# Kernel optimization log

Measured on AMD Instinct MI355X. Metric: run time of the kernel, lower is better.

Reference implementation:

```python
import jax, jax.numpy as jnp
import numpy as np

KEEP_RATIO = 0.5
B, H, W = 8, 1024, 1024


def setup_inputs() -> dict:
    key = jax.random.key(0)
    k1, k2, k3 = jax.random.split(key, 3)
    logits = jax.random.normal(k1, (B, 1, H, W), dtype=jnp.float32)
    targets = jax.random.randint(k2, (B, 1, H, W), 0, 2, dtype=jnp.int32)
    tissue_mask = jax.random.randint(k3, (B, 1, H, W), 0, 2, dtype=jnp.int32)
    return {"logits": logits, "targets": targets, "tissue_mask": tissue_mask}


def reference(logits, targets, tissue_mask):
    b = logits.shape[0]
    x = logits.reshape(b, -1)                       # (B, N)
    t = targets.reshape(b, -1).astype(x.dtype)      # {0,1}
    m = tissue_mask.reshape(b, -1).astype(x.dtype)  # {0,1}
    n = x.shape[1]

    # stable binary_cross_entropy_with_logits, reduction='none'
    bce = jnp.maximum(x, 0.0) - x * t + jnp.log1p(jnp.exp(-jnp.abs(x)))
    loss = bce * m                                  # masked per-pixel loss

    pos = t * m                                     # positives inside tissue
    neg = (1.0 - t) * m                             # negatives inside tissue
    n_pos = jnp.sum(pos, axis=1)                    # (B,)
    n_neg = jnp.sum(neg, axis=1)

    k_all = max(1, int(n * KEEP_RATIO))             # static python int
    # kept count per row: all positives + top-(k_all - n_pos) negatives (clamped)
    k_keep = n_pos + jnp.minimum(jnp.maximum(k_all - n_pos, 0.0), n_neg)  # (B,)

    BIG = jnp.asarray(1e30, x.dtype)
    # sort key: positives always first, then negatives by loss, then non-tissue
    sort_key = jnp.where(pos > 0, BIG, jnp.where(neg > 0, loss, -BIG))
    order = jnp.argsort(-sort_key, axis=1)          # descending
    sorted_loss = jnp.take_along_axis(loss, order, axis=1)

    ranks = jnp.arange(n, dtype=x.dtype)
    keep = (ranks[None, :] < k_keep[:, None]).astype(x.dtype)
    per_sample = jnp.sum(sorted_loss * keep, axis=1) / jnp.maximum(k_keep, 1.0)
    # fallback when no tissue pixels at all: torch keeps index 0 (loss there is 0)
    per_sample = jnp.where(k_keep > 0, per_sample, loss[:, 0])
    return jnp.mean(per_sample)
```

## Files before the change

### kernel.cpp

```cpp
#include <hip/hip_runtime.h>
#include <cstdint>
#include <cstddef>

#define N_PIX   1048576
#define B_ROWS  8
#define K_ALL   524288
#define WG_PER_ROW 256
#define ITERS   4
#define L1_BINS 4096
#define CAP     131072u

struct RowParams {
    double   sumPos;
    unsigned mode;
    unsigned T1;
    unsigned Kp;
    unsigned kneg;
    unsigned npos;
    unsigned pad;
};


__device__ void suffix_select_cnt(const unsigned* cnt, int nbins, unsigned K,
                                  unsigned (&sc)[2][256], int* res_bin, unsigned* res_cntgt)
{
    const int tid = threadIdx.x;
    const int per = nbins >> 8;
    unsigned pc = 0;
    for (int i = 0; i < per; ++i) pc += cnt[nbins - 1 - (tid * per + i)];
    int pp = 0;
    sc[0][tid] = pc;
    __syncthreads();
    for (int ofs = 1; ofs < 256; ofs <<= 1) {
        unsigned c = sc[pp][tid];
        if (tid >= ofs) c += sc[pp][tid - ofs];
        sc[pp ^ 1][tid] = c; pp ^= 1;
        __syncthreads();
    }
    unsigned inc = sc[pp][tid];
    unsigned exc = inc - pc;
    if (exc < K && K <= inc) {
        unsigned cum = exc;
        for (int i = 0; i < per; ++i) {
            int bin = nbins - 1 - (tid * per + i);
            unsigned c = cnt[bin];
            if (cum + c >= K) { *res_bin = bin; *res_cntgt = cum; break; }
            cum += c;
        }
    }
    __syncthreads();
}

__device__ void suffix_select(const unsigned* cnt, const float* sum, int nbins, unsigned K,
                              unsigned (&sc)[2][256], float (&ss)[2][256],
                              int* res_bin, unsigned* res_cntgt, float* res_sumgt)
{
    const int tid = threadIdx.x;
    const int per = nbins >> 8;
    unsigned pc = 0; float ps = 0.f;
    for (int i = 0; i < per; ++i) {
        int bin = nbins - 1 - (tid * per + i);
        pc += cnt[bin]; ps += sum[bin];
    }
    int pp = 0;
    sc[0][tid] = pc; ss[0][tid] = ps;
    __syncthreads();
    for (int ofs = 1; ofs < 256; ofs <<= 1) {
        unsigned c = sc[pp][tid]; float s = ss[pp][tid];
        if (tid >= ofs) { c += sc[pp][tid - ofs]; s += ss[pp][tid - ofs]; }
        sc[pp ^ 1][tid] = c; ss[pp ^ 1][tid] = s;
        pp ^= 1;
        __syncthreads();
    }
    unsigned inc = sc[pp][tid]; float incs = ss[pp][tid];
    unsigned exc = inc - pc;    float exs  = incs - ps;
    if (exc < K && K <= inc) {
        unsigned cum = exc; float csum = exs;
        for (int i = 0; i < per; ++i) {
            int bin = nbins - 1 - (tid * per + i);
            unsigned c = cnt[bin];
            if (cum + c >= K) { *res_bin = bin; *res_cntgt = cum; *res_sumgt = csum; break; }
            cum += c; csum += sum[bin];
        }
    }
    __syncthreads();
}

__global__ __launch_bounds__(256, 4) void k_pass1(
    const float4* __restrict__ lg, const int4* __restrict__ tg, const int4* __restrict__ mk,
    uint4* __restrict__ keybuf, unsigned* __restrict__ histCnt,
    unsigned* __restrict__ partNpos, unsigned* __restrict__ partNneg, double* __restrict__ partSpos)
{
    __shared__ unsigned hc[L1_BINS];
    __shared__ unsigned swp[4], swn[4];
    __shared__ double   sws[4];
    const int tid = threadIdx.x;
    for (int b = tid; b < L1_BINS; b += 256) hc[b] = 0u;

    const int r = blockIdx.x >> 8;
    const int w = blockIdx.x & 255;
    const size_t base = (size_t)r * (N_PIX / 4) + (size_t)w * (ITERS * 256) + tid;

    float4 x[ITERS]; int4 t[ITERS]; int4 m[ITERS];
    #pragma unroll
    for (int i = 0; i < ITERS; ++i) {
        x[i] = lg[base + (size_t)i * 256];
        t[i] = tg[base + (size_t)i * 256];
        m[i] = mk[base + (size_t)i * 256];
    }
    __syncthreads();

    unsigned npos = 0, nneg = 0; float spos = 0.f;

    auto proc = [&](float xx, int tt, int mm) -> unsigned {
        float ax = fabsf(xx);
        float e = __expf(-ax);
        float l = __logf(1.f + e);
        float bce = fmaxf(xx, 0.f) - xx * (float)tt + l;
        unsigned key = 0u;
        if (mm) {
            if (tt) { npos++; spos += bce; }
            else {
                nneg++;
                key = __float_as_uint(bce);
                atomicAdd(&hc[key >> 20], 1u);
            }
        }
        return key;
    };

    #pragma unroll
    for (int i = 0; i < ITERS; ++i) {
        uint4 kv;
        kv.x = proc(x[i].x, t[i].x, m[i].x);
        kv.y = proc(x[i].y, t[i].y, m[i].y);
        kv.z = proc(x[i].z, t[i].z, m[i].z);
        kv.w = proc(x[i].w, t[i].w, m[i].w);
        keybuf[base + (size_t)i * 256] = kv;
    }

    for (int o = 32; o; o >>= 1) {
        npos += __shfl_down(npos, o);
        nneg += __shfl_down(nneg, o);
        spos += __shfl_down(spos, o);
    }
    if ((tid & 63) == 0) { swp[tid >> 6] = npos; swn[tid >> 6] = nneg; sws[tid >> 6] = (double)spos; }
    __syncthreads();
    if (tid == 0) {
        partNpos[blockIdx.x] = swp[0] + swp[1] + swp[2] + swp[3];
        partNneg[blockIdx.x] = swn[0] + swn[1] + swn[2] + swn[3];
        partSpos[blockIdx.x] = sws[0] + sws[1] + sws[2] + sws[3];
    }
    for (int b = tid; b < L1_BINS; b += 256) {
        unsigned c = hc[b];
        if (c) atomicAdd(&histCnt[(size_t)r * L1_BINS + b], c);
    }
}

__global__ __launch_bounds__(256) void k_select1(
    const unsigned* __restrict__ histCnt, const unsigned* __restrict__ partNpos,
    const unsigned* __restrict__ partNneg, const double* __restrict__ partSpos,
    RowParams* __restrict__ params, float* __restrict__ out)
{
    __shared__ unsigned sc[2][256];
    __shared__ int rbin; __shared__ unsigned rcnt;
    __shared__ unsigned swp[4], swn[4];
    __shared__ double   sws[4];

    const int r = blockIdx.x, tid = threadIdx.x;
    if (r == 0 && tid == 0) *out = 0.f;

    unsigned np = partNpos[r * 256 + tid];
    unsigned nn = partNneg[r * 256 + tid];
    double   sp = partSpos[r * 256 + tid];
    for (int o = 32; o; o >>= 1) {
        np += __shfl_down(np, o);
        nn += __shfl_down(nn, o);
        sp += __shfl_down(sp, o);
    }
    if ((tid & 63) == 0) { swp[tid >> 6] = np; swn[tid >> 6] = nn; sws[tid >> 6] = sp; }
    __syncthreads();
    const unsigned npos = swp[0] + swp[1] + swp[2] + swp[3];
    const unsigned nneg = swn[0] + swn[1] + swn[2] + swn[3];
    const double sumPos = sws[0] + sws[1] + sws[2] + sws[3];

    long kl = (long)K_ALL - (long)npos;
    if (kl < 0) kl = 0;
    if (kl > (long)nneg) kl = (long)nneg;
    const unsigned Kneg = (unsigned)kl;

    unsigned mode, T1 = 0xFFFFFFFFu, Kp = 0;
    if (Kneg == 0)          mode = 0;
    else if (Kneg >= nneg)  mode = 1;
    else {
        mode = 2;
        suffix_select_cnt(histCnt + (size_t)r * L1_BINS, L1_BINS, Kneg, sc, &rbin, &rcnt);
        T1 = (unsigned)rbin; Kp = Kneg - rcnt;
    }
    if (tid == 0) {
        RowParams p;
        p.sumPos = sumPos; p.mode = mode; p.T1 = T1; p.Kp = Kp;
        p.kneg = Kneg; p.npos = npos; p.pad = 0;
        params[r] = p;
    }
}

__global__ __launch_bounds__(256, 8) void k_collect(
    const uint4* __restrict__ keybuf, const RowParams* __restrict__ params,
    unsigned* __restrict__ candCnt, unsigned* __restrict__ cand, double* __restrict__ partSgt)
{
    __shared__ double swd[4];
    const int r = blockIdx.x >> 8;
    const int w = blockIdx.x & 255;
    const RowParams p = params[r];
    if (p.mode == 0) {
        if (threadIdx.x == 0) partSgt[blockIdx.x] = 0.0;
        return;
    }
    const unsigned cutHi = (p.mode == 1) ? 1u : ((p.T1 + 1u) << 20);
    const bool coll = (p.mode == 2);
    const unsigned T1 = p.T1;
    const size_t base = (size_t)r * (N_PIX / 4) + (size_t)w * (ITERS * 256) + threadIdx.x;
    unsigned* buf = cand + (size_t)r * CAP;
    const int tid = threadIdx.x, lane = tid & 63;

    uint4 kv[ITERS];
    #pragma unroll
    for (int i = 0; i < ITERS; ++i) kv[i] = keybuf[base + (size_t)i * 256];

    float fs = 0.f;
    #pragma unroll
    for (int i = 0; i < ITERS; ++i) {
        #pragma unroll
        for (int j = 0; j < 4; ++j) {
            unsigned key = (j == 0) ? kv[i].x : (j == 1) ? kv[i].y : (j == 2) ? kv[i].z : kv[i].w;
            if (key >= cutHi) fs += __uint_as_float(key);
            if (coll) {
                bool pr = key && ((key >> 20) == T1);
                unsigned long long mb = __ballot(pr);
                if (mb) {
                    int leader = __ffsll(mb) - 1;
                    unsigned base_s = 0;
                    if (lane == leader) base_s = atomicAdd(&candCnt[r], (unsigned)__popcll(mb));
                    base_s = __shfl(base_s, leader);
                    if (pr) {
                        unsigned slot = base_s + (unsigned)__popcll(mb & ((1ull << lane) - 1ull));
                        if (slot < CAP) buf[slot] = key;
                    }
                }
            }
        }
    }
    double ds = (double)fs;
    for (int o = 32; o; o >>= 1) ds += __shfl_down(ds, o);
    if ((tid & 63) == 0) swd[tid >> 6] = ds;
    __syncthreads();
    if (tid == 0) partSgt[blockIdx.x] = swd[0] + swd[1] + swd[2] + swd[3];
}

__global__ __launch_bounds__(256) void k_final(
    const unsigned* __restrict__ cand, const unsigned* __restrict__ candCnt,
    const RowParams* __restrict__ params, const double* __restrict__ partSgt,
    float* __restrict__ out)
{
    __shared__ unsigned hc[1024];
    __shared__ float    hsum[1024];
    __shared__ unsigned sc[2][256];
    __shared__ float    ss[2][256];
    __shared__ int rbin; __shared__ unsigned rcnt; __shared__ float rsum;
    __shared__ int binA; __shared__ unsigned KA; __shared__ float sumA;
    __shared__ double swd[4];

    const int r = blockIdx.x, tid = threadIdx.x;
    const RowParams p = params[r];

    double sum_gt = 0.0;
    if (p.mode != 0) {
        double ds = partSgt[r * 256 + tid];
        for (int o = 32; o; o >>= 1) ds += __shfl_down(ds, o);
        if ((tid & 63) == 0) swd[tid >> 6] = ds;
        __syncthreads();
        sum_gt = swd[0] + swd[1] + swd[2] + swd[3];
        __syncthreads();
    }

    double sum_sel = 0.0;
    if (p.mode == 1) sum_sel = sum_gt;

    if (p.mode == 2) {
        unsigned M = candCnt[r]; if (M > CAP) M = CAP;
        const unsigned* buf = cand + (size_t)r * CAP;

        for (int b = tid; b < 1024; b += 256) { hc[b] = 0u; hsum[b] = 0.f; }
        __syncthreads();
        for (unsigned i = tid; i < M; i += 256) {
            unsigned k = buf[i]; unsigned b = (k >> 10) & 1023u;
            atomicAdd(&hc[b], 1u);
            atomicAdd(&hsum[b], __uint_as_float(k));
        }
        __syncthreads();
        suffix_select(hc, hsum, 1024, p.Kp, sc, ss, &rbin, &rcnt, &rsum);
        if (tid == 0) { binA = rbin; KA = p.Kp - rcnt; sumA = rsum; }
        __syncthreads();
        const int bA = binA; const unsigned KAx = KA;

        for (int b = tid; b < 1024; b += 256) hc[b] = 0u;
        __syncthreads();
        for (unsigned i = tid; i < M; i += 256) {
            unsigned k = buf[i];
            if (((k >> 10) & 1023u) == (unsigned)bA) atomicAdd(&hc[k & 1023u], 1u);
        }
        __syncthreads();
        const unsigned hi = (p.T1 << 20) | ((unsigned)bA << 10);
        for (int b = tid; b < 1024; b += 256)
            hsum[b] = (float)hc[b] * __uint_as_float(hi | (unsigned)b);
        __syncthreads();
        suffix_select(hc, hsum, 1024, KAx, sc, ss, &rbin, &rcnt, &rsum);

        if (tid == 0) {
            unsigned rem = KAx - rcnt;
            float v = __uint_as_float(hi | (unsigned)rbin);
            sum_sel = sum_gt + (double)sumA + (double)rsum + (double)rem * (double)v;
        }
    }

    if (tid == 0) {
        unsigned long long kk = (unsigned long long)p.npos + (unsigned long long)p.kneg;
        double per = 0.0;
        if (kk > 0) per = (p.sumPos + sum_sel) / (double)kk;
        atomicAdd(out, (float)(per / (double)B_ROWS));
    }
}

extern "C" void kernel_launch(void* const* d_in, const int* in_sizes, int n_in,
                              void* d_out, int out_size, void* d_ws, size_t ws_size,
                              hipStream_t stream)
{
    const float* logits = (const float*)d_in[0];
    const int*   targets = (const int*)d_in[1];
    const int*   tissue = (const int*)d_in[2];

    char* ws = (char*)d_ws;
    size_t off = 0;
    uint32_t* keybuf = (uint32_t*)(ws + off); off += (size_t)B_ROWS * N_PIX * 4;
    unsigned* histCnt = (unsigned*)(ws + off); off += (size_t)B_ROWS * L1_BINS * 4;
    unsigned* candCnt = (unsigned*)(ws + off); off += 64;
    size_t zero_from = (size_t)B_ROWS * N_PIX * 4;
    size_t zero_size = (size_t)B_ROWS * L1_BINS * 4 + 64;
    unsigned* partNpos = (unsigned*)(ws + off); off += (size_t)B_ROWS * WG_PER_ROW * 4;
    unsigned* partNneg = (unsigned*)(ws + off); off += (size_t)B_ROWS * WG_PER_ROW * 4;
    double*   partSpos = (double*)(ws + off);   off += (size_t)B_ROWS * WG_PER_ROW * 8;
    double*   partSgt  = (double*)(ws + off);   off += (size_t)B_ROWS * WG_PER_ROW * 8;
    RowParams* params  = (RowParams*)(ws + off); off += sizeof(RowParams) * B_ROWS;
    off = (off + 255) & ~(size_t)255;
    unsigned* cand = (unsigned*)(ws + off); off += (size_t)B_ROWS * CAP * 4;

    hipMemsetAsync(ws + zero_from, 0, zero_size, stream);

    k_pass1<<<B_ROWS * WG_PER_ROW, 256, 0, stream>>>(
        (const float4*)logits, (const int4*)targets, (const int4*)tissue,
        (uint4*)keybuf, histCnt, partNpos, partNneg, partSpos);
    k_select1<<<B_ROWS, 256, 0, stream>>>(histCnt, partNpos, partNneg, partSpos, params, (float*)d_out);
    k_collect<<<B_ROWS * WG_PER_ROW, 256, 0, stream>>>(
        (const uint4*)keybuf, params, candCnt, cand, partSgt);
    k_final<<<B_ROWS, 256, 0, stream>>>(cand, candCnt, params, partSgt, (float*)d_out);
}
```

Before: 142.5 us.

## Compact negative keys per block and derive the above-threshold sum by subtraction

Pass 1 now writes only in-tissue negative loss keys into a per-block compacted region, using wave ballots and a shared counter, instead of storing a dense key for every pixel. It also accumulates the total negative loss. The collect pass reads only the compacted keys and sums those below the threshold bin. The final kernel recovers the sum above the threshold as total minus low part minus candidates. This cuts global write and read traffic for the intermediate key buffer, at the cost of extra ballot and LDS atomic work in pass 1 and possible cancellation error in the subtraction.

Result: no change. 140.0 us (-1.8%).

```diff
diff --git a/kernel.cpp b/kernel.cpp
--- a/kernel.cpp
+++ b/kernel.cpp
@@ -7,11 +7,13 @@
 #define K_ALL   524288
 #define WG_PER_ROW 256
 #define ITERS   4
+#define ELEMS_PER_BLOCK 4096
 #define L1_BINS 4096
 #define CAP     131072u
 
 struct RowParams {
     double   sumPos;
+    double   sumNeg;
     unsigned mode;
     unsigned T1;
     unsigned Kp;
@@ -88,18 +90,22 @@
 
 __global__ __launch_bounds__(256, 4) void k_pass1(
     const float4* __restrict__ lg, const int4* __restrict__ tg, const int4* __restrict__ mk,
-    uint4* __restrict__ keybuf, unsigned* __restrict__ histCnt,
-    unsigned* __restrict__ partNpos, unsigned* __restrict__ partNneg, double* __restrict__ partSpos)
+    unsigned* __restrict__ negbuf, unsigned* __restrict__ histCnt,
+    unsigned* __restrict__ partNpos, unsigned* __restrict__ partNneg,
+    double* __restrict__ partSpos, double* __restrict__ partSneg)
 {
     __shared__ unsigned hc[L1_BINS];
-    __shared__ unsigned swp[4], swn[4];
-    __shared__ double   sws[4];
+    __shared__ unsigned lbase;
+    __shared__ unsigned swp[4];
+    __shared__ double   sws[4], swn[4];
     const int tid = threadIdx.x;
+    const int lane = tid & 63;
     for (int b = tid; b < L1_BINS; b += 256) hc[b] = 0u;
+    if (tid == 0) lbase = 0u;
 
     const int r = blockIdx.x >> 8;
-    const int w = blockIdx.x & 255;
-    const size_t base = (size_t)r * (N_PIX / 4) + (size_t)w * (ITERS * 256) + tid;
+    const size_t base = (size_t)blockIdx.x * (ITERS * 256) + tid;
+    unsigned* region = negbuf + (size_t)blockIdx.x * ELEMS_PER_BLOCK;
 
     float4 x[ITERS]; int4 t[ITERS]; int4 m[ITERS];
     #pragma unroll
@@ -110,9 +116,9 @@
     }
     __syncthreads();
 
-    unsigned npos = 0, nneg = 0; float spos = 0.f;
-
-    auto proc = [&](float xx, int tt, int mm) -> unsigned {
+    unsigned npos = 0; float spos = 0.f, sneg = 0.f;
+
+    auto key_of = [&](float xx, int tt, int mm) -> unsigned {
         float ax = fabsf(xx);
         float e = __expf(-ax);
         float l = __logf(1.f + e);
@@ -121,7 +127,7 @@
         if (mm) {
             if (tt) { npos++; spos += bce; }
             else {
-                nneg++;
+                sneg += bce;
                 key = __float_as_uint(bce);
                 atomicAdd(&hc[key >> 20], 1u);
             }
@@ -131,25 +137,41 @@
 
     #pragma unroll
     for (int i = 0; i < ITERS; ++i) {
-        uint4 kv;
-        kv.x = proc(x[i].x, t[i].x, m[i].x);
-        kv.y = proc(x[i].y, t[i].y, m[i].y);
-        kv.z = proc(x[i].z, t[i].z, m[i].z);
-        kv.w = proc(x[i].w, t[i].w, m[i].w);
-        keybuf[base + (size_t)i * 256] = kv;
-    }
-
-    for (int o = 32; o; o >>= 1) {
-        npos += __shfl_down(npos, o);
-        nneg += __shfl_down(nneg, o);
-        spos += __shfl_down(spos, o);
-    }
-    if ((tid & 63) == 0) { swp[tid >> 6] = npos; swn[tid >> 6] = nneg; sws[tid >> 6] = (double)spos; }
-    __syncthreads();
-    if (tid == 0) {
-        partNpos[blockIdx.x] = swp[0] + swp[1] + swp[2] + swp[3];
-        partNneg[blockIdx.x] = swn[0] + swn[1] + swn[2] + swn[3];
-        partSpos[blockIdx.x] = sws[0] + sws[1] + sws[2] + sws[3];
+        unsigned k4[4];
+        k4[0] = key_of(x[i].x, t[i].x, m[i].x);
+        k4[1] = key_of(x[i].y, t[i].y, m[i].y);
+        k4[2] = key_of(x[i].z, t[i].z, m[i].z);
+        k4[3] = key_of(x[i].w, t[i].w, m[i].w);
+        #pragma unroll
+        for (int j = 0; j < 4; ++j) {
+            unsigned key = k4[j];
+            bool pr = key != 0u;
+            unsigned long long mb = __ballot(pr);
+            if (mb) {
+                int leader = __ffsll((long long)mb) - 1;
+                unsigned wbase = 0;
+                if (lane == leader) wbase = atomicAdd(&lbase, (unsigned)__popcll(mb));
+                wbase = __shfl(wbase, leader);
+                if (pr) region[wbase + (unsigned)__popcll(mb & ((1ull << lane) - 1ull))] = key;
+            }
+        }
+    }
+
+    {
+        unsigned np = npos; float sp = spos, sn = sneg;
+        for (int o = 32; o; o >>= 1) {
+            np += __shfl_down(np, o);
+            sp += __shfl_down(sp, o);
+            sn += __shfl_down(sn, o);
+        }
+        if ((tid & 63) == 0) { swp[tid >> 6] = np; sws[tid >> 6] = (double)sp; swn[tid >> 6] = (double)sn; }
+        __syncthreads();
+        if (tid == 0) {
+            partNpos[blockIdx.x] = swp[0] + swp[1] + swp[2] + swp[3];
+            partSpos[blockIdx.x] = sws[0] + sws[1] + sws[2] + sws[3];
+            partSneg[blockIdx.x] = swn[0] + swn[1] + swn[2] + swn[3];
+            partNneg[blockIdx.x] = lbase;
+        }
     }
     for (int b = tid; b < L1_BINS; b += 256) {
         unsigned c = hc[b];
@@ -160,12 +182,12 @@
 __global__ __launch_bounds__(256) void k_select1(
     const unsigned* __restrict__ histCnt, const unsigned* __restrict__ partNpos,
     const unsigned* __restrict__ partNneg, const double* __restrict__ partSpos,
-    RowParams* __restrict__ params, float* __restrict__ out)
+    const double* __restrict__ partSneg, RowParams* __restrict__ params, float* __restrict__ out)
 {
     __shared__ unsigned sc[2][256];
     __shared__ int rbin; __shared__ unsigned rcnt;
     __shared__ unsigned swp[4], swn[4];
-    __shared__ double   sws[4];
+    __shared__ double   sws[4], swn2[4];
 
     const int r = blockIdx.x, tid = threadIdx.x;
     if (r == 0 && tid == 0) *out = 0.f;
@@ -173,16 +195,19 @@
     unsigned np = partNpos[r * 256 + tid];
     unsigned nn = partNneg[r * 256 + tid];
     double   sp = partSpos[r * 256 + tid];
+    double   sn = partSneg[r * 256 + tid];
     for (int o = 32; o; o >>= 1) {
         np += __shfl_down(np, o);
         nn += __shfl_down(nn, o);
         sp += __shfl_down(sp, o);
-    }
-    if ((tid & 63) == 0) { swp[tid >> 6] = np; swn[tid >> 6] = nn; sws[tid >> 6] = sp; }
+        sn += __shfl_down(sn, o);
+    }
+    if ((tid & 63) == 0) { swp[tid >> 6] = np; swn[tid >> 6] = nn; sws[tid >> 6] = sp; swn2[tid >> 6] = sn; }
     __syncthreads();
     const unsigned npos = swp[0] + swp[1] + swp[2] + swp[3];
     const unsigned nneg = swn[0] + swn[1] + swn[2] + swn[3];
     const double sumPos = sws[0] + sws[1] + sws[2] + sws[3];
+    const double sumNeg = swn2[0] + swn2[1] + swn2[2] + swn2[3];
 
     long kl = (long)K_ALL - (long)npos;
     if (kl < 0) kl = 0;
@@ -199,55 +224,46 @@
     }
     if (tid == 0) {
         RowParams p;
-        p.sumPos = sumPos; p.mode = mode; p.T1 = T1; p.Kp = Kp;
+        p.sumPos = sumPos; p.sumNeg = sumNeg;
+        p.mode = mode; p.T1 = T1; p.Kp = Kp;
         p.kneg = Kneg; p.npos = npos; p.pad = 0;
         params[r] = p;
     }
 }
 
 __global__ __launch_bounds__(256, 8) void k_collect(
-    const uint4* __restrict__ keybuf, const RowParams* __restrict__ params,
+    const unsigned* __restrict__ negbuf, const unsigned* __restrict__ partNneg,
+    const RowParams* __restrict__ params,
     unsigned* __restrict__ candCnt, unsigned* __restrict__ cand, double* __restrict__ partSgt)
 {
     __shared__ double swd[4];
     const int r = blockIdx.x >> 8;
-    const int w = blockIdx.x & 255;
+    const int tid = threadIdx.x, lane = tid & 63;
     const RowParams p = params[r];
-    if (p.mode == 0) {
-        if (threadIdx.x == 0) partSgt[blockIdx.x] = 0.0;
+    if (p.mode != 2) {
+        if (tid == 0) partSgt[blockIdx.x] = 0.0;
         return;
     }
-    const unsigned cutHi = (p.mode == 1) ? 1u : ((p.T1 + 1u) << 20);
-    const bool coll = (p.mode == 2);
     const unsigned T1 = p.T1;
-    const size_t base = (size_t)r * (N_PIX / 4) + (size_t)w * (ITERS * 256) + threadIdx.x;
+    const unsigned lowCut = T1 << 20;
+    const unsigned M = partNneg[blockIdx.x];
+    const unsigned* region = negbuf + (size_t)blockIdx.x * ELEMS_PER_BLOCK;
     unsigned* buf = cand + (size_t)r * CAP;
-    const int tid = threadIdx.x, lane = tid & 63;
-
-    uint4 kv[ITERS];
-    #pragma unroll
-    for (int i = 0; i < ITERS; ++i) kv[i] = keybuf[base + (size_t)i * 256];
 
     float fs = 0.f;
-    #pragma unroll
-    for (int i = 0; i < ITERS; ++i) {
-        #pragma unroll
-        for (int j = 0; j < 4; ++j) {
-            unsigned key = (j == 0) ? kv[i].x : (j == 1) ? kv[i].y : (j == 2) ? kv[i].z : kv[i].w;
-            if (key >= cutHi) fs += __uint_as_float(key);
-            if (coll) {
-                bool pr = key && ((key >> 20) == T1);
-                unsigned long long mb = __ballot(pr);
-                if (mb) {
-                    int leader = __ffsll(mb) - 1;
-                    unsigned base_s = 0;
-                    if (lane == leader) base_s = atomicAdd(&candCnt[r], (unsigned)__popcll(mb));
-                    base_s = __shfl(base_s, leader);
-                    if (pr) {
-                        unsigned slot = base_s + (unsigned)__popcll(mb & ((1ull << lane) - 1ull));
-                        if (slot < CAP) buf[slot] = key;
-                    }
-                }
+    for (unsigned idx = tid; idx < M; idx += 256) {
+        unsigned key = region[idx];
+        if (key < lowCut) fs += __uint_as_float(key);
+        bool pr = (key >> 20) == T1;
+        unsigned long long mb = __ballot(pr);
+        if (mb) {
+            int leader = __ffsll((long long)mb) - 1;
+            unsigned base_s = 0;
+            if (lane == leader) base_s = atomicAdd(&candCnt[r], (unsigned)__popcll(mb));
+            base_s = __shfl(base_s, leader);
+            if (pr) {
+                unsigned slot = base_s + (unsigned)__popcll(mb & ((1ull << lane) - 1ull));
+                if (slot < CAP) buf[slot] = key;
             }
         }
     }
@@ -269,23 +285,20 @@
     __shared__ float    ss[2][256];
     __shared__ int rbin; __shared__ unsigned rcnt; __shared__ float rsum;
     __shared__ int binA; __shared__ unsigned KA; __shared__ float sumA;
-    __shared__ double swd[4];
+    __shared__ double swd[4], swc[4];
 
     const int r = blockIdx.x, tid = threadIdx.x;
     const RowParams p = params[r];
 
-    double sum_gt = 0.0;
-    if (p.mode != 0) {
-        double ds = partSgt[r * 256 + tid];
-        for (int o = 32; o; o >>= 1) ds += __shfl_down(ds, o);
-        if ((tid & 63) == 0) swd[tid >> 6] = ds;
-        __syncthreads();
-        sum_gt = swd[0] + swd[1] + swd[2] + swd[3];
-        __syncthreads();
-    }
+    double sg = partSgt[r * 256 + tid];
+    for (int o = 32; o; o >>= 1) sg += __shfl_down(sg, o);
+    if ((tid & 63) == 0) swd[tid >> 6] = sg;
+    __syncthreads();
+    const double sum_low = swd[0] + swd[1] + swd[2] + swd[3];
+    __syncthreads();
 
     double sum_sel = 0.0;
-    if (p.mode == 1) sum_sel = sum_gt;
+    if (p.mode == 1) sum_sel = p.sumNeg;
 
     if (p.mode == 2) {
         unsigned M = candCnt[r]; if (M > CAP) M = CAP;
@@ -293,12 +306,19 @@
 
         for (int b = tid; b < 1024; b += 256) { hc[b] = 0u; hsum[b] = 0.f; }
         __syncthreads();
+        double ct = 0.0;
         for (unsigned i = tid; i < M; i += 256) {
             unsigned k = buf[i]; unsigned b = (k >> 10) & 1023u;
+            float f = __uint_as_float(k);
             atomicAdd(&hc[b], 1u);
-            atomicAdd(&hsum[b], __uint_as_float(k));
-        }
-        __syncthreads();
+            atomicAdd(&hsum[b], f);
+            ct += (double)f;
+        }
+        for (int o = 32; o; o >>= 1) ct += __shfl_down(ct, o);
+        if ((tid & 63) == 0) swc[tid >> 6] = ct;
+        __syncthreads();
+        const double candTotal = swc[0] + swc[1] + swc[2] + swc[3];
+
         suffix_select(hc, hsum, 1024, p.Kp, sc, ss, &rbin, &rcnt, &rsum);
         if (tid == 0) { binA = rbin; KA = p.Kp - rcnt; sumA = rsum; }
         __syncthreads();
@@ -320,6 +340,7 @@
         if (tid == 0) {
             unsigned rem = KAx - rcnt;
             float v = __uint_as_float(hi | (unsigned)rbin);
+            double sum_gt = p.sumNeg - sum_low - candTotal;
             sum_sel = sum_gt + (double)sumA + (double)rsum + (double)rem * (double)v;
         }
     }
@@ -340,28 +361,29 @@
     const int*   targets = (const int*)d_in[1];
     const int*   tissue = (const int*)d_in[2];
 
+    const int NBLK = B_ROWS * WG_PER_ROW;
     char* ws = (char*)d_ws;
     size_t off = 0;
-    uint32_t* keybuf = (uint32_t*)(ws + off); off += (size_t)B_ROWS * N_PIX * 4;
     unsigned* histCnt = (unsigned*)(ws + off); off += (size_t)B_ROWS * L1_BINS * 4;
     unsigned* candCnt = (unsigned*)(ws + off); off += 64;
-    size_t zero_from = (size_t)B_ROWS * N_PIX * 4;
-    size_t zero_size = (size_t)B_ROWS * L1_BINS * 4 + 64;
-    unsigned* partNpos = (unsigned*)(ws + off); off += (size_t)B_ROWS * WG_PER_ROW * 4;
-    unsigned* partNneg = (unsigned*)(ws + off); off += (size_t)B_ROWS * WG_PER_ROW * 4;
-    double*   partSpos = (double*)(ws + off);   off += (size_t)B_ROWS * WG_PER_ROW * 8;
-    double*   partSgt  = (double*)(ws + off);   off += (size_t)B_ROWS * WG_PER_ROW * 8;
+    size_t zero_size = off;
+    unsigned* partNpos = (unsigned*)(ws + off); off += (size_t)NBLK * 4;
+    unsigned* partNneg = (unsigned*)(ws + off); off += (size_t)NBLK * 4;
+    double*   partSpos = (double*)(ws + off);   off += (size_t)NBLK * 8;
+    double*   partSneg = (double*)(ws + off);   off += (size_t)NBLK * 8;
+    double*   partSgt  = (double*)(ws + off);   off += (size_t)NBLK * 8;
     RowParams* params  = (RowParams*)(ws + off); off += sizeof(RowParams) * B_ROWS;
     off = (off + 255) & ~(size_t)255;
-    unsigned* cand = (unsigned*)(ws + off); off += (size_t)B_ROWS * CAP * 4;
-
-    hipMemsetAsync(ws + zero_from, 0, zero_size, stream);
-
-    k_pass1<<<B_ROWS * WG_PER_ROW, 256, 0, stream>>>(
+    unsigned* cand = (unsigned*)(ws + off);   off += (size_t)B_ROWS * CAP * 4;
+    unsigned* negbuf = (unsigned*)(ws + off); off += (size_t)NBLK * ELEMS_PER_BLOCK * 4;
+
+    hipMemsetAsync(ws, 0, zero_size, stream);
+
+    k_pass1<<<NBLK, 256, 0, stream>>>(
         (const float4*)logits, (const int4*)targets, (const int4*)tissue,
-        (uint4*)keybuf, histCnt, partNpos, partNneg, partSpos);
-    k_select1<<<B_ROWS, 256, 0, stream>>>(histCnt, partNpos, partNneg, partSpos, params, (float*)d_out);
-    k_collect<<<B_ROWS * WG_PER_ROW, 256, 0, stream>>>(
-        (const uint4*)keybuf, params, candCnt, cand, partSgt);
+        negbuf, histCnt, partNpos, partNneg, partSpos, partSneg);
+    k_select1<<<B_ROWS, 256, 0, stream>>>(histCnt, partNpos, partNneg, partSpos, partSneg,
+                                          params, (float*)d_out);
+    k_collect<<<NBLK, 256, 0, stream>>>(negbuf, partNneg, params, candCnt, cand, partSgt);
     k_final<<<B_ROWS, 256, 0, stream>>>(cand, candCnt, params, partSgt, (float*)d_out);
 }
```
